# Performance work log

Measured on AMD Instinct MI355X. Metric: run time of the kernel, lower is better.

## Reference

```python
import jax, jax.numpy as jnp
import numpy as np
import math

D_MODEL = 1024
NUM_HEADS = 16
D_K = D_MODEL // NUM_HEADS
MAX_LEN = 2048
B, S = 2, 1024


def setup_inputs() -> dict:
    key = jax.random.key(0)
    ks = jax.random.split(key, 10)
    lin_scale = 1.0 / math.sqrt(D_MODEL)
    # torch Linear: weight (out, in), y = x @ W.T + b
    Wq = jax.random.uniform(ks[0], (D_MODEL, D_MODEL), jnp.float32, -lin_scale, lin_scale)
    Wk = jax.random.uniform(ks[1], (D_MODEL, D_MODEL), jnp.float32, -lin_scale, lin_scale)
    Wv = jax.random.uniform(ks[2], (D_MODEL, D_MODEL), jnp.float32, -lin_scale, lin_scale)
    Wo = jax.random.uniform(ks[3], (D_MODEL, D_MODEL), jnp.float32, -lin_scale, lin_scale)
    bq = jnp.zeros((D_MODEL,), jnp.float32)
    bk = jnp.zeros((D_MODEL,), jnp.float32)
    bv = jnp.zeros((D_MODEL,), jnp.float32)
    bo = jnp.zeros((D_MODEL,), jnp.float32)
    # xavier_uniform for Er (max_len, d_k)
    er_bound = math.sqrt(6.0 / (MAX_LEN + D_K))
    Er = jax.random.uniform(ks[4], (MAX_LEN, D_K), jnp.float32, -er_bound, er_bound)
    x = jax.random.normal(ks[5], (B, S, D_MODEL), jnp.float32)
    return {"x": x, "Wq": Wq, "bq": bq, "Wk": Wk, "bk": bk,
            "Wv": Wv, "bv": bv, "Wo": Wo, "bo": bo, "Er": Er}


def reference(x, Wq, bq, Wk, bk, Wv, bv, Wo, bo, Er):
    Bsz, Slen, Dm = x.shape
    H, dk = NUM_HEADS, D_K

    def proj(W, b):
        y = jnp.einsum('bsd,ed->bse', x, W) + b
        return y.reshape(Bsz, Slen, H, dk).transpose(0, 2, 1, 3)  # (B,H,S,dk)

    Q = proj(Wq, bq)
    K = proj(Wk, bk)
    V = proj(Wv, bv)

    # content-content scores
    AC = jnp.einsum('bhid,bhjd->bhij', Q, K)  # (B,H,S,S)

    # relative position embeddings for distances S-1 .. -(S-1)
    rel_pos = jnp.arange(Slen - 1, -Slen, -1)  # (2S-1,)
    idx = rel_pos + (Slen - 1)                 # map to 0..2S-2 (requires 2S-1 <= max_len)
    Er_emb = Er[idx]                           # (2S-1, dk)
    BD_full = jnp.einsum('bhid,md->bhim', Q, Er_emb)  # (B,H,S,2S-1)

    # relative shift: final[i,j] = BD_full[i, S-1 - i + j] (column for distance i-j)
    i_idx = jnp.arange(Slen)[:, None]                  # (S,1)
    m_idx = (Slen - 1) - i_idx + jnp.arange(Slen)[None, :]  # (S,S)
    BD = BD_full[:, :, i_idx, m_idx]                   # (B,H,S,S)

    scores = (AC + BD) / math.sqrt(dk)
    attn = jax.nn.softmax(scores, axis=-1)  # dropout is identity at eval
    out = jnp.einsum('bhij,bhjd->bhid', attn, V)       # (B,H,S,dk)
    out = out.transpose(0, 2, 1, 3).reshape(Bsz, Slen, Dm)
    return jnp.einsum('bsd,ed->bse', out, Wo) + bo
```

## Files before the change

kernel.cpp:

```cpp
#include <hip/hip_runtime.h>
#include <hip/hip_bf16.h>
#include <math.h>

#define D_MODEL 1024
#define NUM_HEADS 16
#define D_K 64
#define SEQ 1024
#define BATCH 2

typedef __hip_bfloat16 bf16;
typedef __bf16 bf16x8 __attribute__((ext_vector_type(8)));
typedef __bf16 bf16x4 __attribute__((ext_vector_type(4)));
typedef float floatx4 __attribute__((ext_vector_type(4)));

__device__ __forceinline__ floatx4 mfma16(bf16x8 a, bf16x8 b, floatx4 c) {
    return __builtin_amdgcn_mfma_f32_16x16x32_bf16(a, b, c, 0, 0, 0);
}

__device__ __forceinline__ void gl_lds16(const bf16* g, __bf16* l) {
    __builtin_amdgcn_global_load_lds(
        (const __attribute__((address_space(1))) void*)g,
        (__attribute__((address_space(3))) void*)l, 16, 0, 0);
}

struct ConvSrcs { const void* p[10]; };

__global__ __launch_bounds__(256) void convert_all_kernel(ConvSrcs srcs,
                                                          bf16* __restrict__ dstbase,
                                                          int* __restrict__ flagg) {
    __shared__ int cnt[256];
    const int tid = threadIdx.x;
    {
        const float* xf = (const float*)srcs.p[0];
        int sane = 0;
#pragma unroll
        for (int i = 0; i < 4; ++i) {
            const float v = xf[tid * 4 + i];
            const float a = fabsf(v);
            if (v == 0.0f || (a > 1e-8f && a < 1e8f)) sane++;
        }
        cnt[tid] = sane;
    }
    __syncthreads();
    for (int s = 128; s > 0; s >>= 1) {
        if (tid < s) cnt[tid] += cnt[tid + s];
        __syncthreads();
    }
    const int flag = (cnt[0] > 922) ? 1 : 0;
    if (blockIdx.x == 0 && tid == 0) flagg[0] = flag;

    const long long e = ((long long)blockIdx.x * 256 + tid) * 8;
    int seg; long long base;
    if      (e < 2097152LL) { seg = 0; base = 0; }
    else if (e < 3145728LL) { seg = 1; base = 2097152LL; }
    else if (e < 4194304LL) { seg = 2; base = 3145728LL; }
    else if (e < 5242880LL) { seg = 3; base = 4194304LL; }
    else if (e < 6291456LL) { seg = 4; base = 5242880LL; }
    else if (e < 6292480LL) { seg = 5; base = 6291456LL; }
    else if (e < 6293504LL) { seg = 6; base = 6292480LL; }
    else if (e < 6294528LL) { seg = 7; base = 6293504LL; }
    else if (e < 6295552LL) { seg = 8; base = 6294528LL; }
    else                    { seg = 9; base = 6295552LL; }
    const long long local = e - base;
    __bf16 tmp[8];
    if (flag) {
        const float* s = (const float*)srcs.p[seg] + local;
#pragma unroll
        for (int t = 0; t < 8; ++t) tmp[t] = (__bf16)s[t];
        *(bf16x8*)(void*)(dstbase + e) = *(const bf16x8*)tmp;
    } else {
        *(bf16x8*)(void*)(dstbase + e) =
            *(const bf16x8*)(const void*)((const bf16*)srcs.p[seg] + local);
    }
}

__global__ __launch_bounds__(256, 2) void gemm_qkv_kernel(const bf16* __restrict__ x,
        const bf16* __restrict__ Wq, const bf16* __restrict__ Wk, const bf16* __restrict__ Wv,
        const bf16* __restrict__ bq, const bf16* __restrict__ bk, const bf16* __restrict__ bv,
        bf16* __restrict__ Qb, bf16* __restrict__ Kb, bf16* __restrict__ Vt) {
    const int wsel = blockIdx.x >> 3;
    const int n0 = (blockIdx.x & 7) * 128;
    const int m0 = blockIdx.y * 128;
    const bf16* W    = (wsel == 0) ? Wq : ((wsel == 1) ? Wk : Wv);
    const bf16* bias = (wsel == 0) ? bq : ((wsel == 1) ? bk : bv);

    __shared__ __bf16 smem[128 * 128 * 2];
    __bf16* As = smem;
    __bf16* Bs = smem + 16384;

    const int tid = threadIdx.x;
    const int wave = tid >> 6, lane = tid & 63, quad = lane >> 4, l16 = lane & 15;
    const int wr = (wave >> 1) * 64, wc = (wave & 1) * 64;
    const int lrow = lane >> 4;
    const int lcg  = lane & 15;

    floatx4 acc[4][4];
#pragma unroll
    for (int r = 0; r < 4; ++r)
#pragma unroll
        for (int c = 0; c < 4; ++c) acc[r][c] = (floatx4)0.f;

    for (int k0 = 0; k0 < 1024; k0 += 128) {
        __syncthreads();
#pragma unroll
        for (int i = 0; i < 8; ++i) {
            const int ci = wave * 8 + i;
            const int grow = ci * 4 + lrow;
            const int gcg = lcg ^ (grow & 15);
            gl_lds16(x + (size_t)(m0 + grow) * 1024 + k0 + gcg * 8, As + ci * 512);
            gl_lds16(W + (size_t)(n0 + grow) * 1024 + k0 + gcg * 8, Bs + ci * 512);
        }
        __syncthreads();
#pragma unroll
        for (int kk = 0; kk < 4; ++kk) {
            const int sg = ((kk * 4 + quad) ^ l16) * 8;
            bf16x8 af[4], bfr[4];
#pragma unroll
            for (int r = 0; r < 4; ++r)
                af[r] = *(const bf16x8*)&As[(wr + r * 16 + l16) * 128 + sg];
#pragma unroll
            for (int c = 0; c < 4; ++c)
                bfr[c] = *(const bf16x8*)&Bs[(wc + c * 16 + l16) * 128 + sg];
#pragma unroll
            for (int r = 0; r < 4; ++r)
#pragma unroll
                for (int c = 0; c < 4; ++c)
                    acc[r][c] = mfma16(af[r], bfr[c], acc[r][c]);
        }
    }

    if (wsel < 2) {
        bf16* Cb = (wsel == 0) ? Qb : Kb;
#pragma unroll
        for (int c = 0; c < 4; ++c) {
            const int col = n0 + wc + c * 16 + l16;
            const float bvl = (float)bias[col];
#pragma unroll
            for (int r = 0; r < 4; ++r)
#pragma unroll
                for (int v = 0; v < 4; ++v) {
                    const int row = m0 + wr + r * 16 + quad * 4 + v;
                    Cb[(size_t)row * 1024 + col] = (bf16)(acc[r][c][v] + bvl);
                }
        }
    } else {
        __bf16* Ls = smem;
        __syncthreads();
#pragma unroll
        for (int c = 0; c < 4; ++c) {
            const int col = wc + c * 16 + l16;
            const float bvl = (float)bias[n0 + col];
#pragma unroll
            for (int r = 0; r < 4; ++r)
#pragma unroll
                for (int v = 0; v < 4; ++v) {
                    const int row = wr + r * 16 + quad * 4 + v;
                    Ls[col * 132 + row] = (__bf16)(acc[r][c][v] + bvl);
                }
        }
        __syncthreads();
        const int b = m0 >> 10, s0 = m0 & 1023, h0 = n0 >> 6;
        const int d = tid >> 1, sg2 = (tid & 1) * 64;
        bf16* g = Vt + ((size_t)((b * NUM_HEADS + h0 + (d >> 6)) * 64 + (d & 63))) * SEQ
                  + s0 + sg2;
#pragma unroll
        for (int c = 0; c < 64; c += 8)
            *(bf16x8*)(void*)(g + c) = *(const bf16x8*)&Ls[d * 132 + sg2 + c];
    }
}

__global__ __launch_bounds__(256, 3) void attn_mfma_kernel(const bf16* __restrict__ Q,
                                                           const bf16* __restrict__ Kc,
                                                           const bf16* __restrict__ Vt,
                                                           const bf16* __restrict__ Er,
                                                           bf16* __restrict__ Opart,
                                                           float* __restrict__ Ml) {
    const int i0 = blockIdx.x * 128;
    const int h = blockIdx.y;
    const int zz = blockIdx.z;
    const int b = zz / 3, jsel = zz - b * 3;
    const int tid = threadIdx.x;
    const int wave = tid >> 6, lane = tid & 63, quad = lane >> 4, l16 = lane & 15;

    const int jbeg = (jsel == 0) ? 0 : ((jsel == 1) ? 384 : 704);
    const int nt   = (jsel == 0) ? 6 : 5;

    __shared__ __bf16 Ks[64][72];
    __shared__ __bf16 Vs[80][72];
    __shared__ __bf16 scr_all[4][3264];
    __bf16* scr = &scr_all[wave][0];
    __bf16* Qs = &scr_all[0][0];

    for (int e = tid; e < 16 * 72; e += 256) {
        const int r = e / 72, c = e - r * 72;
        Vs[64 + r][c] = (r == 0) ? (__bf16)1.0f : (__bf16)0.0f;
    }
    {
        const int r = tid >> 1, cg = (tid & 1) * 32;
        const bf16* g = Q + ((size_t)(b * SEQ + i0 + r)) * D_MODEL + h * 64 + cg;
#pragma unroll
        for (int c = 0; c < 32; c += 8)
            *(bf16x8*)(void*)(Qs + r * 72 + cg + c) = *(const bf16x8*)(const void*)(g + c);
    }
    __syncthreads();
    bf16x8 aq[2][2];
#pragma unroll
    for (int half = 0; half < 2; ++half)
#pragma unroll
        for (int kk = 0; kk < 2; ++kk)
            aq[half][kk] = *(const bf16x8*)(const void*)(
                Qs + (wave * 32 + half * 16 + l16) * 72 + kk * 32 + quad * 8);

    floatx4 oacc[5][2];
#pragma unroll
    for (int ct = 0; ct < 5; ++ct)
#pragma unroll
        for (int half = 0; half < 2; ++half) oacc[ct][half] = (floatx4)0.f;

    const int eb = 960 + i0;
    const bf16* Kg = Kc + (size_t)b * SEQ * D_MODEL + h * 64;
    const bf16* Vtg = Vt + (size_t)((b * NUM_HEADS + h) * 64) * SEQ;

    const int r4 = tid >> 2, c4 = (tid & 3) * 16;
    bf16x8 kp0, kp1, vp0, vp1;
    {
        const bf16* kg = Kg + (size_t)(jbeg + r4) * D_MODEL + c4;
        const bf16* vg = Vtg + (size_t)r4 * SEQ + jbeg + c4;
        kp0 = *(const bf16x8*)(const void*)kg;
        kp1 = *(const bf16x8*)(const void*)(kg + 8);
        vp0 = *(const bf16x8*)(const void*)vg;
        vp1 = *(const bf16x8*)(const void*)(vg + 8);
    }

    for (int t = 0; t < nt; ++t) {
        const int j0 = jbeg + t * 64;
        __syncthreads();
        *(bf16x8*)&Ks[r4][c4]     = kp0;
        *(bf16x8*)&Ks[r4][c4 + 8] = kp1;
        *(bf16x8*)&Vs[r4][c4]     = vp0;
        *(bf16x8*)&Vs[r4][c4 + 8] = vp1;
        __syncthreads();
        if (t < nt - 1) {
            const int jn = j0 + 64;
            const bf16* kg = Kg + (size_t)(jn + r4) * D_MODEL + c4;
            const bf16* vg = Vtg + (size_t)r4 * SEQ + jn + c4;
            kp0 = *(const bf16x8*)(const void*)kg;
            kp1 = *(const bf16x8*)(const void*)(kg + 8);
            vp0 = *(const bf16x8*)(const void*)vg;
            vp1 = *(const bf16x8*)(const void*)(vg + 8);
        }

#pragma unroll
        for (int ct = 0; ct < 6; ++ct) {
            const int erow = eb - j0 + wave * 32 + ct * 16 + l16;
            const bf16* ep = Er + (size_t)erow * 64 + quad * 8;
            bf16x8 be0 = *(const bf16x8*)(const void*)ep;
            bf16x8 be1 = *(const bf16x8*)(const void*)(ep + 32);
#pragma unroll
            for (int half = 0; half < 2; ++half) {
                floatx4 tv = (floatx4)0.f;
                tv = mfma16(aq[half][0], be0, tv);
                tv = mfma16(aq[half][1], be1, tv);
                bf16x4 tb;
#pragma unroll
                for (int v = 0; v < 4; ++v) tb[v] = (__bf16)tv[v];
                *(bf16x4*)(void*)(scr + (ct * 16 + l16) * 34 + half * 16 + quad * 4) = tb;
            }
        }
        floatx4 sfrag[4][2];
#pragma unroll
        for (int ct = 0; ct < 4; ++ct) {
            bf16x8 bk0 = *(const bf16x8*)&Ks[ct * 16 + l16][quad * 8];
            bf16x8 bk1 = *(const bf16x8*)&Ks[ct * 16 + l16][32 + quad * 8];
#pragma unroll
            for (int half = 0; half < 2; ++half) {
                floatx4 s = (floatx4)0.f;
                s = mfma16(aq[half][0], bk0, s);
                s = mfma16(aq[half][1], bk1, s);
                sfrag[ct][half] = s;
            }
        }
#pragma unroll
        for (int ct = 0; ct < 4; ++ct)
#pragma unroll
            for (int half = 0; half < 2; ++half)
#pragma unroll
                for (int v = 0; v < 4; ++v) {
                    const int rl = half * 16 + quad * 4 + v;
                    const int cl = 63 + rl - (ct * 16 + l16);
                    sfrag[ct][half][v] =
                        (sfrag[ct][half][v] + (float)scr[cl * 34 + rl]) * 0.125f;
                }
#pragma unroll
        for (int ct = 0; ct < 4; ++ct)
#pragma unroll
            for (int half = 0; half < 2; ++half)
#pragma unroll
                for (int v = 0; v < 4; ++v) {
                    const int rl = half * 16 + quad * 4 + v;
                    scr[rl * 72 + ct * 16 + l16] = (__bf16)__expf(sfrag[ct][half][v]);
                }
        bf16x8 ap[2][2];
#pragma unroll
        for (int half = 0; half < 2; ++half)
#pragma unroll
            for (int kk = 0; kk < 2; ++kk)
                ap[half][kk] = *(const bf16x8*)(const void*)(
                    scr + (half * 16 + l16) * 72 + kk * 32 + quad * 8);
#pragma unroll
        for (int ct = 0; ct < 5; ++ct) {
            bf16x8 bv0 = *(const bf16x8*)&Vs[ct * 16 + l16][quad * 8];
            bf16x8 bv1 = *(const bf16x8*)&Vs[ct * 16 + l16][32 + quad * 8];
#pragma unroll
            for (int half = 0; half < 2; ++half) {
                oacc[ct][half] = mfma16(ap[half][0], bv0, oacc[ct][half]);
                oacc[ct][half] = mfma16(ap[half][1], bv1, oacc[ct][half]);
            }
        }
    }

    bf16* Op = Opart + (size_t)jsel * 2097152;
#pragma unroll
    for (int ct = 0; ct < 4; ++ct)
#pragma unroll
        for (int half = 0; half < 2; ++half)
#pragma unroll
            for (int v = 0; v < 4; ++v) {
                const int row = i0 + wave * 32 + half * 16 + quad * 4 + v;
                const int col = h * 64 + ct * 16 + l16;
                Op[((size_t)(b * SEQ + row)) * D_MODEL + col] = (bf16)oacc[ct][half][v];
            }
    if (l16 == 0) {
        const int base = ((jsel * 2 + b) * 16 + h) * 1024;
#pragma unroll
        for (int half = 0; half < 2; ++half)
#pragma unroll
            for (int v = 0; v < 4; ++v) {
                const int ig = i0 + wave * 32 + half * 16 + quad * 4 + v;
                Ml[base + ig] = oacc[4][half][v];
            }
    }
}

__global__ __launch_bounds__(256) void combine_kernel(const bf16* __restrict__ Opart,
                                                      const float* __restrict__ Ml,
                                                      bf16* __restrict__ Ob) {
    const int e = (blockIdx.x * 256 + threadIdx.x) * 8;
    const int row = e >> 10;
    const int b = row >> 10, i = row & 1023;
    const int h = (e & 1023) >> 6;
    float l = 0.f;
#pragma unroll
    for (int s = 0; s < 3; ++s) l += Ml[(((s * 2 + b) * 16 + h) << 10) + i];
    const float inv = 1.0f / l;
    bf16x8 o1 = *(const bf16x8*)(const void*)(Opart + e);
    bf16x8 o2 = *(const bf16x8*)(const void*)(Opart + 2097152 + e);
    bf16x8 o3 = *(const bf16x8*)(const void*)(Opart + 4194304 + e);
    bf16x8 o;
#pragma unroll
    for (int v = 0; v < 8; ++v)
        o[v] = (__bf16)(((float)o1[v] + (float)o2[v] + (float)o3[v]) * inv);
    *(bf16x8*)(void*)(Ob + e) = o;
}

__global__ __launch_bounds__(256) void gemm_out_kernel(const bf16* __restrict__ A,
        const bf16* __restrict__ W, const bf16* __restrict__ bias,
        void* __restrict__ C, const int* __restrict__ flag) {
    const int n0 = blockIdx.x * 64;
    const int m0 = blockIdx.y * 64;
    __shared__ __bf16 smem[64 * 128 * 2];
    __bf16* As = smem;
    __bf16* Bs = smem + 8192;
    const int tid = threadIdx.x;
    const int wave = tid >> 6, lane = tid & 63, quad = lane >> 4, l16 = lane & 15;
    const int wr = (wave >> 1) * 32, wc = (wave & 1) * 32;
    const int lrow = lane >> 4, lcg = lane & 15;

    floatx4 acc[2][2];
#pragma unroll
    for (int r = 0; r < 2; ++r)
#pragma unroll
        for (int c = 0; c < 2; ++c) acc[r][c] = (floatx4)0.f;

    for (int k0 = 0; k0 < 1024; k0 += 128) {
        __syncthreads();
#pragma unroll
        for (int i = 0; i < 4; ++i) {
            const int ci = wave * 4 + i;
            const int grow = ci * 4 + lrow;
            const int gcg = lcg ^ (grow & 15);
            gl_lds16(A + (size_t)(m0 + grow) * 1024 + k0 + gcg * 8, As + ci * 512);
            gl_lds16(W + (size_t)(n0 + grow) * 1024 + k0 + gcg * 8, Bs + ci * 512);
        }
        __syncthreads();
#pragma unroll
        for (int kk = 0; kk < 4; ++kk) {
            bf16x8 af[2], bfr[2];
            const int sg = ((kk * 4 + quad) ^ l16) * 8;
#pragma unroll
            for (int r = 0; r < 2; ++r)
                af[r] = *(const bf16x8*)&As[(wr + r * 16 + l16) * 128 + sg];
#pragma unroll
            for (int c = 0; c < 2; ++c)
                bfr[c] = *(const bf16x8*)&Bs[(wc + c * 16 + l16) * 128 + sg];
#pragma unroll
            for (int r = 0; r < 2; ++r)
#pragma unroll
                for (int c = 0; c < 2; ++c)
                    acc[r][c] = mfma16(af[r], bfr[c], acc[r][c]);
        }
    }
#pragma unroll
    for (int c = 0; c < 2; ++c) {
        const int col = n0 + wc + c * 16 + l16;
        const float bvl = (float)bias[col];
#pragma unroll
        for (int r = 0; r < 2; ++r)
#pragma unroll
            for (int v = 0; v < 4; ++v) {
                const int row = m0 + wr + r * 16 + quad * 4 + v;
                const float val = acc[r][c][v] + bvl;
                const size_t idx = (size_t)row * 1024 + col;
                if (*flag) ((float*)C)[idx] = val;
                else       ((bf16*)C)[idx] = (bf16)val;
            }
    }
}

extern "C" void kernel_launch(void* const* d_in, const int* in_sizes, int n_in,
                              void* d_out, int out_size, void* d_ws, size_t ws_size,
                              hipStream_t stream) {
    const size_t E_X = 2097152;
    const size_t E_CANON = 6426624;

    char* ws = (char*)d_ws;
    int* flag = (int*)ws;
    bf16* canon = (bf16*)(ws + 16);
    bf16* xc  = canon;
    bf16* Wqc = canon + 2097152;
    bf16* Wkc = canon + 3145728;
    bf16* Wvc = canon + 4194304;
    bf16* Woc = canon + 5242880;
    bf16* bqc = canon + 6291456;
    bf16* bkc = canon + 6292480;
    bf16* bvc = canon + 6293504;
    bf16* boc = canon + 6294528;
    bf16* Erc = canon + 6295552;
    bf16* p = canon + E_CANON;
    bf16* Qb    = p;  p += E_X;
    bf16* Kb    = p;  p += E_X;
    bf16* Vt    = p;  p += E_X;
    bf16* Opart = p;  p += 3 * E_X;
    float* Ml   = (float*)p;

    ConvSrcs cs;
    cs.p[0] = d_in[0]; cs.p[1] = d_in[1]; cs.p[2] = d_in[3]; cs.p[3] = d_in[5];
    cs.p[4] = d_in[7]; cs.p[5] = d_in[2]; cs.p[6] = d_in[4]; cs.p[7] = d_in[6];
    cs.p[8] = d_in[8]; cs.p[9] = d_in[9];
    convert_all_kernel<<<3138, 256, 0, stream>>>(cs, canon, flag);

    gemm_qkv_kernel<<<dim3(24, 16), 256, 0, stream>>>(xc, Wqc, Wkc, Wvc,
                                                      bqc, bkc, bvc, Qb, Kb, Vt);

    attn_mfma_kernel<<<dim3(8, 16, 6), 256, 0, stream>>>(Qb, Kb, Vt, Erc, Opart, Ml);

    combine_kernel<<<1024, 256, 0, stream>>>(Opart, Ml, Qb);

    gemm_out_kernel<<<dim3(16, 32), 256, 0, stream>>>(Qb, Woc, boc, d_out, flag);
}
```

Measured before the change: 177.7 us.

## Fuse fp32-to-bf16 input conversion into GEMM tile loads, drop convert kernel

Removes the standalone conversion kernel that rewrote x and all weights to bf16 in workspace. The QKV and output GEMMs now probe the input dtype themselves and convert fp32 tiles to bf16 while staging them into LDS. The Er conversion is folded into the Q-projection blocks. This saves one launch and a full read/write pass over about 6M elements. In exchange the fp32 path uses plain register loads instead of direct global-to-LDS loads, and every block repeats the flag reduction.

```diff
diff --git a/kernel.cpp b/kernel.cpp
--- a/kernel.cpp
+++ b/kernel.cpp
@@ -23,66 +23,42 @@
         (__attribute__((address_space(3))) void*)l, 16, 0, 0);
 }
 
-struct ConvSrcs { const void* p[10]; };
-
-__global__ __launch_bounds__(256) void convert_all_kernel(ConvSrcs srcs,
-                                                          bf16* __restrict__ dstbase,
-                                                          int* __restrict__ flagg) {
-    __shared__ int cnt[256];
+__device__ __forceinline__ bf16x8 cvt8(const float* s) {
+    bf16x8 o;
+#pragma unroll
+    for (int t = 0; t < 8; ++t) o[t] = (__bf16)s[t];
+    return o;
+}
+
+__device__ __forceinline__ int probe_flag(const void* xr, int* cnt) {
     const int tid = threadIdx.x;
-    {
-        const float* xf = (const float*)srcs.p[0];
-        int sane = 0;
-#pragma unroll
-        for (int i = 0; i < 4; ++i) {
-            const float v = xf[tid * 4 + i];
-            const float a = fabsf(v);
-            if (v == 0.0f || (a > 1e-8f && a < 1e8f)) sane++;
-        }
-        cnt[tid] = sane;
-    }
+    const float* xf = (const float*)xr;
+    int sane = 0;
+#pragma unroll
+    for (int i = 0; i < 4; ++i) {
+        const float v = xf[tid * 4 + i];
+        const float a = fabsf(v);
+        if (v == 0.0f || (a > 1e-8f && a < 1e8f)) sane++;
+    }
+    cnt[tid] = sane;
     __syncthreads();
     for (int s = 128; s > 0; s >>= 1) {
         if (tid < s) cnt[tid] += cnt[tid + s];
         __syncthreads();
     }
-    const int flag = (cnt[0] > 922) ? 1 : 0;
-    if (blockIdx.x == 0 && tid == 0) flagg[0] = flag;
-
-    const long long e = ((long long)blockIdx.x * 256 + tid) * 8;
-    int seg; long long base;
-    if      (e < 2097152LL) { seg = 0; base = 0; }
-    else if (e < 3145728LL) { seg = 1; base = 2097152LL; }
-    else if (e < 4194304LL) { seg = 2; base = 3145728LL; }
-    else if (e < 5242880LL) { seg = 3; base = 4194304LL; }
-    else if (e < 6291456LL) { seg = 4; base = 5242880LL; }
-    else if (e < 6292480LL) { seg = 5; base = 6291456LL; }
-    else if (e < 6293504LL) { seg = 6; base = 6292480LL; }
-    else if (e < 6294528LL) { seg = 7; base = 6293504LL; }
-    else if (e < 6295552LL) { seg = 8; base = 6294528LL; }
-    else                    { seg = 9; base = 6295552LL; }
-    const long long local = e - base;
-    __bf16 tmp[8];
-    if (flag) {
-        const float* s = (const float*)srcs.p[seg] + local;
-#pragma unroll
-        for (int t = 0; t < 8; ++t) tmp[t] = (__bf16)s[t];
-        *(bf16x8*)(void*)(dstbase + e) = *(const bf16x8*)tmp;
-    } else {
-        *(bf16x8*)(void*)(dstbase + e) =
-            *(const bf16x8*)(const void*)((const bf16*)srcs.p[seg] + local);
-    }
-}
-
-__global__ __launch_bounds__(256, 2) void gemm_qkv_kernel(const bf16* __restrict__ x,
-        const bf16* __restrict__ Wq, const bf16* __restrict__ Wk, const bf16* __restrict__ Wv,
-        const bf16* __restrict__ bq, const bf16* __restrict__ bk, const bf16* __restrict__ bv,
+    return (cnt[0] > 922) ? 1 : 0;
+}
+
+__global__ __launch_bounds__(256, 2) void gemm_qkv_kernel(const void* __restrict__ xr,
+        const void* __restrict__ Wqr, const void* __restrict__ Wkr, const void* __restrict__ Wvr,
+        const void* __restrict__ bqr, const void* __restrict__ bkr, const void* __restrict__ bvr,
+        const void* __restrict__ Err, bf16* __restrict__ Erc,
         bf16* __restrict__ Qb, bf16* __restrict__ Kb, bf16* __restrict__ Vt) {
     const int wsel = blockIdx.x >> 3;
     const int n0 = (blockIdx.x & 7) * 128;
     const int m0 = blockIdx.y * 128;
-    const bf16* W    = (wsel == 0) ? Wq : ((wsel == 1) ? Wk : Wv);
-    const bf16* bias = (wsel == 0) ? bq : ((wsel == 1) ? bk : bv);
+    const void* Wr = (wsel == 0) ? Wqr : ((wsel == 1) ? Wkr : Wvr);
+    const void* br = (wsel == 0) ? bqr : ((wsel == 1) ? bkr : bvr);
 
     __shared__ __bf16 smem[128 * 128 * 2];
     __bf16* As = smem;
@@ -91,8 +67,9 @@
     const int tid = threadIdx.x;
     const int wave = tid >> 6, lane = tid & 63, quad = lane >> 4, l16 = lane & 15;
     const int wr = (wave >> 1) * 64, wc = (wave & 1) * 64;
-    const int lrow = lane >> 4;
-    const int lcg  = lane & 15;
+    const int lrow = lane >> 4, lcg = lane & 15;
+
+    const int flagv = probe_flag(xr, (int*)smem);
 
     floatx4 acc[4][4];
 #pragma unroll
@@ -102,13 +79,26 @@
 
     for (int k0 = 0; k0 < 1024; k0 += 128) {
         __syncthreads();
-#pragma unroll
-        for (int i = 0; i < 8; ++i) {
-            const int ci = wave * 8 + i;
-            const int grow = ci * 4 + lrow;
-            const int gcg = lcg ^ (grow & 15);
-            gl_lds16(x + (size_t)(m0 + grow) * 1024 + k0 + gcg * 8, As + ci * 512);
-            gl_lds16(W + (size_t)(n0 + grow) * 1024 + k0 + gcg * 8, Bs + ci * 512);
+        if (flagv) {
+#pragma unroll
+            for (int i = 0; i < 8; ++i) {
+                const int ci = wave * 8 + i;
+                const int grow = ci * 4 + lrow;
+                const int gcg = lcg ^ (grow & 15);
+                const float* xs = (const float*)xr + (size_t)(m0 + grow) * 1024 + k0 + gcg * 8;
+                const float* ws = (const float*)Wr + (size_t)(n0 + grow) * 1024 + k0 + gcg * 8;
+                *(bf16x8*)&As[ci * 512 + lane * 8] = cvt8(xs);
+                *(bf16x8*)&Bs[ci * 512 + lane * 8] = cvt8(ws);
+            }
+        } else {
+#pragma unroll
+            for (int i = 0; i < 8; ++i) {
+                const int ci = wave * 8 + i;
+                const int grow = ci * 4 + lrow;
+                const int gcg = lcg ^ (grow & 15);
+                gl_lds16((const bf16*)xr + (size_t)(m0 + grow) * 1024 + k0 + gcg * 8, As + ci * 512);
+                gl_lds16((const bf16*)Wr + (size_t)(n0 + grow) * 1024 + k0 + gcg * 8, Bs + ci * 512);
+            }
         }
         __syncthreads();
 #pragma unroll
@@ -134,7 +124,7 @@
 #pragma unroll
         for (int c = 0; c < 4; ++c) {
             const int col = n0 + wc + c * 16 + l16;
-            const float bvl = (float)bias[col];
+            const float bvl = flagv ? ((const float*)br)[col] : (float)((const bf16*)br)[col];
 #pragma unroll
             for (int r = 0; r < 4; ++r)
 #pragma unroll
@@ -143,13 +133,27 @@
                     Cb[(size_t)row * 1024 + col] = (bf16)(acc[r][c][v] + bvl);
                 }
         }
+        if (wsel == 0) {
+            const long long eoff = (long long)(blockIdx.x * 16 + blockIdx.y) * 1024 + tid * 4;
+            if (flagv) {
+                const float* s = (const float*)Err + eoff;
+                bf16x4 o;
+#pragma unroll
+                for (int v = 0; v < 4; ++v) o[v] = (__bf16)s[v];
+                *(bf16x4*)(void*)(Erc + eoff) = o;
+            } else {
+                *(bf16x4*)(void*)(Erc + eoff) =
+                    *(const bf16x4*)(const void*)((const bf16*)Err + eoff);
+            }
+        }
     } else {
         __bf16* Ls = smem;
         __syncthreads();
 #pragma unroll
         for (int c = 0; c < 4; ++c) {
             const int col = wc + c * 16 + l16;
-            const float bvl = (float)bias[n0 + col];
+            const float bvl = flagv ? ((const float*)br)[n0 + col]
+                                    : (float)((const bf16*)br)[n0 + col];
 #pragma unroll
             for (int r = 0; r < 4; ++r)
 #pragma unroll
@@ -364,8 +368,8 @@
 }
 
 __global__ __launch_bounds__(256) void gemm_out_kernel(const bf16* __restrict__ A,
-        const bf16* __restrict__ W, const bf16* __restrict__ bias,
-        void* __restrict__ C, const int* __restrict__ flag) {
+        const void* __restrict__ Wr, const void* __restrict__ br,
+        void* __restrict__ C, const void* __restrict__ xr) {
     const int n0 = blockIdx.x * 64;
     const int m0 = blockIdx.y * 64;
     __shared__ __bf16 smem[64 * 128 * 2];
@@ -376,6 +380,8 @@
     const int wr = (wave >> 1) * 32, wc = (wave & 1) * 32;
     const int lrow = lane >> 4, lcg = lane & 15;
 
+    const int flagv = probe_flag(xr, (int*)smem);
+
     floatx4 acc[2][2];
 #pragma unroll
     for (int r = 0; r < 2; ++r)
@@ -390,7 +396,13 @@
             const int grow = ci * 4 + lrow;
             const int gcg = lcg ^ (grow & 15);
             gl_lds16(A + (size_t)(m0 + grow) * 1024 + k0 + gcg * 8, As + ci * 512);
-            gl_lds16(W + (size_t)(n0 + grow) * 1024 + k0 + gcg * 8, Bs + ci * 512);
+            if (flagv) {
+                const float* ws = (const float*)Wr + (size_t)(n0 + grow) * 1024 + k0 + gcg * 8;
+                *(bf16x8*)&Bs[ci * 512 + lane * 8] = cvt8(ws);
+            } else {
+                gl_lds16((const bf16*)Wr + (size_t)(n0 + grow) * 1024 + k0 + gcg * 8,
+                         Bs + ci * 512);
+            }
         }
         __syncthreads();
 #pragma unroll
@@ -413,7 +425,7 @@
 #pragma unroll
     for (int c = 0; c < 2; ++c) {
         const int col = n0 + wc + c * 16 + l16;
-        const float bvl = (float)bias[col];
+        const float bvl = flagv ? ((const float*)br)[col] : (float)((const bf16*)br)[col];
 #pragma unroll
         for (int r = 0; r < 2; ++r)
 #pragma unroll
@@ -421,7 +433,7 @@
                 const int row = m0 + wr + r * 16 + quad * 4 + v;
                 const float val = acc[r][c][v] + bvl;
                 const size_t idx = (size_t)row * 1024 + col;
-                if (*flag) ((float*)C)[idx] = val;
+                if (flagv) ((float*)C)[idx] = val;
                 else       ((bf16*)C)[idx] = (bf16)val;
             }
     }
@@ -431,40 +443,24 @@
                               void* d_out, int out_size, void* d_ws, size_t ws_size,
                               hipStream_t stream) {
     const size_t E_X = 2097152;
-    const size_t E_CANON = 6426624;
+    const size_t E_ER = 131072;
 
     char* ws = (char*)d_ws;
-    int* flag = (int*)ws;
-    bf16* canon = (bf16*)(ws + 16);
-    bf16* xc  = canon;
-    bf16* Wqc = canon + 2097152;
-    bf16* Wkc = canon + 3145728;
-    bf16* Wvc = canon + 4194304;
-    bf16* Woc = canon + 5242880;
-    bf16* bqc = canon + 6291456;
-    bf16* bkc = canon + 6292480;
-    bf16* bvc = canon + 6293504;
-    bf16* boc = canon + 6294528;
-    bf16* Erc = canon + 6295552;
-    bf16* p = canon + E_CANON;
+    bf16* p = (bf16*)(ws + 16);
+    bf16* Erc   = p;  p += E_ER;
     bf16* Qb    = p;  p += E_X;
     bf16* Kb    = p;  p += E_X;
     bf16* Vt    = p;  p += E_X;
     bf16* Opart = p;  p += 3 * E_X;
     float* Ml   = (float*)p;
 
-    ConvSrcs cs;
-    cs.p[0] = d_in[0]; cs.p[1] = d_in[1]; cs.p[2] = d_in[3]; cs.p[3] = d_in[5];
-    cs.p[4] = d_in[7]; cs.p[5] = d_in[2]; cs.p[6] = d_in[4]; cs.p[7] = d_in[6];
-    cs.p[8] = d_in[8]; cs.p[9] = d_in[9];
-    convert_all_kernel<<<3138, 256, 0, stream>>>(cs, canon, flag);
-
-    gemm_qkv_kernel<<<dim3(24, 16), 256, 0, stream>>>(xc, Wqc, Wkc, Wvc,
-                                                      bqc, bkc, bvc, Qb, Kb, Vt);
+    gemm_qkv_kernel<<<dim3(24, 16), 256, 0, stream>>>(
+        d_in[0], d_in[1], d_in[3], d_in[5], d_in[2], d_in[4], d_in[6],
+        d_in[9], Erc, Qb, Kb, Vt);
 
     attn_mfma_kernel<<<dim3(8, 16, 6), 256, 0, stream>>>(Qb, Kb, Vt, Erc, Opart, Ml);
 
     combine_kernel<<<1024, 256, 0, stream>>>(Opart, Ml, Qb);
 
-    gemm_out_kernel<<<dim3(16, 32), 256, 0, stream>>>(Qb, Woc, boc, d_out, flag);
-}
+    gemm_out_kernel<<<dim3(16, 32), 256, 0, stream>>>(Qb, d_in[7], d_in[8], d_out, d_in[0]);
+}
```

Result: slower. 187.2 us (+5.4%).
